# Kernel optimization log

Measured on AMD Instinct MI355X. Metric: run time of the kernel, lower is better.

## Reference

```python
import jax, jax.numpy as jnp
import numpy as np

B, TIN, NB, H, SOUT, R, G = 64, 49, 24, 384, 10, 2, 5  # batch, in_frames, bones, hidden, out_frames, rec_steps, gates(i,fs,ft,o,c)


def setup_inputs() -> dict:
    key = jax.random.key(0)
    ks = jax.random.split(key, 9)
    s = 1.0 / np.sqrt(H)  # scaled init so gates don't saturate (original uses randn)
    return {
        "hidden_states": jax.random.normal(ks[0], (B, TIN, NB, H), jnp.float32),
        "cell_states": jax.random.normal(ks[1], (B, TIN, NB, H), jnp.float32),
        "global_t_state": jax.random.normal(ks[2], (B, NB, H), jnp.float32),
        "global_s_state": jax.random.normal(ks[3], (B, TIN, H), jnp.float32),
        "p": jax.random.normal(ks[4], (B, SOUT, NB, H), jnp.float32),
        # per (rec_step, bone) cell weights: x / h_temporal / h_spatial projections for 5 gates
        "U": jax.random.normal(ks[5], (R, NB, G, H, H), jnp.float32) * s,
        "Wt": jax.random.normal(ks[6], (R, NB, G, H, H), jnp.float32) * s,
        "Ws": jax.random.normal(ks[7], (R, NB, G, H, H), jnp.float32) * s,
        "b": jax.random.normal(ks[8], (R, NB, G, H), jnp.float32) * s,
    }


def _cell(Ub, Wtb, Wsb, bb, x, ht, hs, ct, cs):
    # Ub/Wtb/Wsb: [G,H,H], bb: [G,H]; x/ht/hs/ct/cs: [B,H]
    g = (jnp.einsum('bh,ghk->bgk', x, Ub)
         + jnp.einsum('bh,ghk->bgk', ht, Wtb)
         + jnp.einsum('bh,ghk->bgk', hs, Wsb) + bb)
    i_n = jax.nn.sigmoid(g[:, 0])
    f_s = jax.nn.sigmoid(g[:, 1])
    f_t = jax.nn.sigmoid(g[:, 2])
    o_n = jax.nn.sigmoid(g[:, 3])
    c_n = jnp.tanh(g[:, 4])
    c_h = i_n * c_n + f_t * ct + f_s * cs
    return o_n * jnp.tanh(c_h), c_h


def reference(hidden_states, cell_states, global_t_state, global_s_state, p, U, Wt, Ws, b):
    # rec step 0: h_t = h_s = hidden_states; rec step 1: h_t = cat(global_t, hidden), h_s = hidden
    h_t1 = jnp.concatenate([global_t_state[:, None], hidden_states], axis=1)
    hm = hidden_states.mean(axis=(1, 2))                    # [B,H] spatial boundary (bone 0) for both steps
    cm = cell_states.mean(axis=(1, 2))
    bound_h = jnp.stack([hm, hm])                            # [R,B,H]
    bound_c = jnp.stack([cm, cm])
    h_prev = jnp.stack([hidden_states.mean(1), h_t1.mean(1)])  # [R,B,NB,H] frame-0 row (bones 1:)
    c_prev = jnp.stack([cell_states.mean(1)] * 2)

    Un, Wtn, Wsn, bn = (jnp.swapaxes(a, 0, 1) for a in (U, Wt, Ws, b))  # [NB,R,...]

    def frame_step(carry, p_f):  # p_f: [NB,B,H]
        h_prev, c_prev = carry                              # [R,B,NB,H]
        hp_n = jnp.moveaxis(h_prev, 2, 0)                   # [NB,R,B,H]
        cp_n = jnp.moveaxis(c_prev, 2, 0)

        def bone_step(bc, xs):
            hl, cl = bc                                     # [R,B,H] left-neighbor (spatial) state
            Ub, Wtb, Wsb, bb, x0, hp, cp = xs
            h0, c0 = _cell(Ub[0], Wtb[0], Wsb[0], bb[0], x0, hp[0], hl[0], cp[0], cl[0])
            h1, c1 = _cell(Ub[1], Wtb[1], Wsb[1], bb[1], h0, hp[1], hl[1], cp[1], cl[1])
            hn = jnp.stack([h0, h1])
            cn = jnp.stack([c0, c1])
            return (hn, cn), (hn, cn)

        _, (hs_all, cs_all) = jax.lax.scan(
            bone_step, (bound_h, bound_c), (Un, Wtn, Wsn, bn, p_f, hp_n, cp_n))
        h_new = jnp.moveaxis(hs_all, 0, 2)                  # [R,B,NB,H]
        c_new = jnp.moveaxis(cs_all, 0, 2)
        return (h_new, c_new), (h_new[-1], c_new[-1])

    p_frames = jnp.transpose(p, (1, 2, 0, 3))               # [SOUT,NB,B,H]
    _, (h_out, c_out) = jax.lax.scan(frame_step, (h_prev, c_prev), p_frames)
    return jnp.moveaxis(h_out, 0, 1), jnp.moveaxis(c_out, 0, 1)  # [B,SOUT,NB,H] each
```

## Files before the change

### kernel.cpp

```cpp
#include <hip/hip_runtime.h>

#define BATCH 64
#define TIN   49
#define NB    24
#define HID   384
#define SOUT  10
#define NGATE 5

typedef __attribute__((ext_vector_type(4))) float f32x4;
typedef __attribute__((ext_vector_type(8))) short short8v;

__device__ __forceinline__ unsigned short f2bf(float f) {
    union { float f; unsigned u; } v; v.f = f;
    unsigned r = v.u + 0x7fffu + ((v.u >> 16) & 1u);
    return (unsigned short)(r >> 16);
}
__device__ __forceinline__ float bf2f(unsigned short h) {
    union { unsigned u; float f; } v; v.u = ((unsigned)h) << 16; return v.f;
}

#define NW3_BLK 4320
#define NP_BLK  23040
#define NM_BLK  576

__global__ __launch_bounds__(256) void prologue_kernel(
    const float* __restrict__ U, const float* __restrict__ Wt,
    const float* __restrict__ Ws, const float* __restrict__ p,
    const float* __restrict__ hid, const float* __restrict__ cel,
    const float* __restrict__ gt,
    unsigned short* __restrict__ wpack, unsigned short* __restrict__ pb,
    unsigned short* __restrict__ hp_b, float* __restrict__ cp_f)
{
    __shared__ unsigned short tile[64][390];
    int bx = blockIdx.x;
    if (bx < NW3_BLK) {
        int q = bx;
        int kb = q % 6; q /= 6;
        int m  = q % 3; q /= 3;
        int g  = q % 5; q /= 5;
        int cell = q;
        const float* W = (m == 0) ? U : (m == 1) ? Wt : Ws;
        const float* src = W + ((size_t)(cell * NGATE + g) * HID + kb * 64) * HID;
        int tid = threadIdx.x;
#pragma unroll
        for (int i = 0; i < 24; ++i) {
            int c = tid + i * 256;
            int row = c / 96, c4 = (c % 96) * 4;
            float4 v = *(const float4*)(src + (size_t)row * HID + c4);
            tile[row][c4 + 0] = f2bf(v.x);
            tile[row][c4 + 1] = f2bf(v.y);
            tile[row][c4 + 2] = f2bf(v.z);
            tile[row][c4 + 3] = f2bf(v.w);
        }
        __syncthreads();
        int lane = tid & 63, grp = tid >> 6;
#pragma unroll
        for (int uu = 0; uu < 12; ++uu) {
            int unit = grp * 12 + uu;
            int pair = unit & 1, kc2 = (unit >> 1) & 1, t32 = unit >> 2;
            int kl = kc2 * 32 + (lane >> 4) * 8;
            int cl = t32 * 32 + pair * 16 + (lane & 15);
            unsigned short o[8];
#pragma unroll
            for (int jj = 0; jj < 8; ++jj) o[jj] = tile[kl + jj][cl];
            int kc = m * 12 + kb * 2 + kc2;
            size_t dst = ((size_t)((cell * 12 + t32) * NGATE + g) * 72
                          + kc * 2 + pair) * 64 + lane;
            *(short8v*)(wpack + dst * 8) = *(const short8v*)o;
        }
    } else if (bx < NW3_BLK + NP_BLK) {
        size_t idx = (size_t)(bx - NW3_BLK) * 256 + threadIdx.x;
        int h = (int)(idx % HID);
        size_t q = idx / HID;
        int b = (int)(q % BATCH); q /= BATCH;
        int n = (int)(q % NB); q /= NB;
        int f = (int)q;
        pb[idx] = f2bf(p[((size_t)(b * SOUT + f) * NB + n) * HID + h]);
    } else {
        int idx = (bx - NW3_BLK - NP_BLK) * 256 + threadIdx.x;
        const int total4 = NB * BATCH * HID / 4;
        if (idx >= total4) return;
        const int H4 = HID / 4;
        int h = (idx % H4) * 4;
        int b = (idx / H4) % BATCH;
        int n = idx / (H4 * BATCH);
        const int fs4 = NB * HID / 4;
        const float4* ph = (const float4*)(hid + ((size_t)b * TIN * NB + n) * HID + h);
        const float4* pc = (const float4*)(cel + ((size_t)b * TIN * NB + n) * HID + h);
        float sh[4] = {0,0,0,0}, sc[4] = {0,0,0,0};
        for (int t = 0; t < TIN; ++t) {
            float4 vh = ph[(size_t)t * fs4];
            float4 vc = pc[(size_t)t * fs4];
            sh[0] += vh.x; sh[1] += vh.y; sh[2] += vh.z; sh[3] += vh.w;
            sc[0] += vc.x; sc[1] += vc.y; sc[2] += vc.z; sc[3] += vc.w;
        }
        float4 g4 = *(const float4*)(gt + ((size_t)b * NB + n) * HID + h);
        const float* g_ = (const float*)&g4;
        unsigned short o0[4], o1[4];
        float c0[4];
#pragma unroll
        for (int j = 0; j < 4; ++j) {
            o0[j] = f2bf(sh[j] / TIN);
            o1[j] = f2bf((g_[j] + sh[j]) / (TIN + 1));
            c0[j] = sc[j] / TIN;
        }
        size_t base = (size_t)idx * 4;
        const size_t tot = (size_t)NB * BATCH * HID;
        *(uint2*)(hp_b + base)       = *(const uint2*)o0;
        *(uint2*)(hp_b + tot + base) = *(const uint2*)o1;
        *(float4*)(cp_f + base)       = make_float4(c0[0], c0[1], c0[2], c0[3]);
        *(float4*)(cp_f + tot + base) = make_float4(c0[0], c0[1], c0[2], c0[3]);
    }
}

__global__ void init_bounds_kernel(const unsigned short* __restrict__ hp_b,
                                   const float* __restrict__ cp_f,
                                   unsigned short* __restrict__ bh_b,
                                   float* __restrict__ bc_f) {
    int idx = blockIdx.x * blockDim.x + threadIdx.x;
    if (idx >= BATCH * HID) return;
    float sh = 0.f, sc = 0.f;
    for (int n = 0; n < NB; ++n) {
        sh += bf2f(hp_b[(size_t)n * BATCH * HID + idx]);
        sc += cp_f[(size_t)n * BATCH * HID + idx];
    }
    bh_b[idx] = f2bf(sh / NB);
    bc_f[idx] = sc / NB;
}

union SMem {
    unsigned short A[3][64][392];
    float gl[3][NGATE][64][35];
};

__global__ __launch_bounds__(960) void cell_fused_kernel(
    int d, int A0,
    const unsigned short* __restrict__ pb,
    const unsigned short* __restrict__ wpack,
    const float* __restrict__ bias,
    const unsigned short* __restrict__ hp_b,
    const float* __restrict__ cp_f,
    const unsigned short* __restrict__ bh_b,
    const float* __restrict__ bc_f,
    unsigned short* __restrict__ h_sl,
    float* __restrict__ c_sl,
    float* __restrict__ out)
{
    __shared__ SMem sm;

    int y = blockIdx.y;
    int rstep, dg;
    if (y < A0) { rstep = 0; dg = d; }
    else        { rstep = 1; dg = d - 1; y -= A0; }
    int lo = dg - (SOUT - 1); if (lo < 0) lo = 0;
    const int n = lo + y;
    const int f = dg - n;
    const int cur = dg & 1, prv = cur ^ 1;
    const int t = blockIdx.x;
    const int wv   = threadIdx.x >> 6;
    const int gate = wv % NGATE;
    const int m    = wv / NGATE;
    const int lane = threadIdx.x & 63;
    const int S = BATCH * HID;
    const int cell = rstep * NB + n;

    const unsigned short *xb, *htb, *hsb;
    const float *ctb, *csb;
    if (rstep == 0) {
        xb  = pb + (size_t)(f * NB + n) * S;
        htb = f ? h_sl + (size_t)((prv * 2 + 0) * NB + n) * S : hp_b + (size_t)n * S;
        hsb = n ? h_sl + (size_t)((prv * 2 + 0) * NB + n - 1) * S : bh_b;
        ctb = f ? c_sl + (size_t)((prv * 2 + 0) * NB + n) * S : cp_f + (size_t)n * S;
        csb = n ? c_sl + (size_t)((prv * 2 + 0) * NB + n - 1) * S : bc_f;
    } else {
        xb  = h_sl + (size_t)((cur * 2 + 0) * NB + n) * S;
        htb = f ? h_sl + (size_t)((prv * 2 + 1) * NB + n) * S
                : hp_b + (size_t)(NB + n) * S;
        hsb = n ? h_sl + (size_t)((prv * 2 + 1) * NB + n - 1) * S : bh_b;
        ctb = f ? c_sl + (size_t)((prv * 2 + 1) * NB + n) * S
                : cp_f + (size_t)(NB + n) * S;
        csb = n ? c_sl + (size_t)((prv * 2 + 1) * NB + n - 1) * S : bc_f;
    }

    const short8v* wp = (const short8v*)wpack
        + (size_t)((cell * 12 + t) * NGATE + gate) * (36 * 2 * 64);
    const short8v* wbm = wp + (size_t)(m * 24) * 64 + lane;

    const int eb = threadIdx.x & 63;
    const int ecq = (threadIdx.x >> 6) & 3;
    float4 cth[2], csh[2];
    if (threadIdx.x < 256) {
#pragma unroll
        for (int h = 0; h < 2; ++h) {
            int colg = t * 32 + h * 16 + ecq * 4;
            cth[h] = *(const float4*)(ctb + (size_t)eb * HID + colg);
            csh[h] = *(const float4*)(csb + (size_t)eb * HID + colg);
        }
    }

    const int tid = threadIdx.x;
    uint4 streg[12];
#pragma unroll
    for (int s = 0; s < 3; ++s) {
        const unsigned short* sp = (s == 0) ? xb : (s == 1) ? htb : hsb;
#pragma unroll
        for (int i = 0; i < 4; ++i) {
            int c = tid + i * 960;
            if (i < 3 || c < 3072) {
                int row = c / 48, cc = c - row * 48;
                streg[s * 4 + i] = *(const uint4*)(sp + (size_t)row * HID + cc * 8);
            }
        }
    }
#pragma unroll
    for (int s = 0; s < 3; ++s) {
#pragma unroll
        for (int i = 0; i < 4; ++i) {
            int c = tid + i * 960;
            if (i < 3 || c < 3072) {
                int row = c / 48, cc = c - row * 48;
                *(uint4*)&sm.A[s][row][cc * 8] = streg[s * 4 + i];
            }
        }
    }

    short8v bufB[3][2];
#pragma unroll
    for (int j = 0; j < 3; ++j) {
        bufB[j][0] = wbm[(size_t)j * 128];
        bufB[j][1] = wbm[(size_t)j * 128 + 64];
    }
    __syncthreads();

    f32x4 acc[2][4];
#pragma unroll
    for (int pr = 0; pr < 2; ++pr)
#pragma unroll
        for (int q = 0; q < 4; ++q) acc[pr][q] = (f32x4){0, 0, 0, 0};

    const int arow = lane & 15;
    const int akg  = (lane >> 4) * 8;

#pragma unroll
    for (int j = 0; j < 12; ++j) {
        const int koff = j * 32 + akg;
        short8v a[4];
#pragma unroll
        for (int q = 0; q < 4; ++q)
            a[q] = *(const short8v*)&sm.A[m][arow + q * 16][koff];
        const int sl = j % 3;
#pragma unroll
        for (int q = 0; q < 4; ++q) {
            acc[0][q] = __builtin_amdgcn_mfma_f32_16x16x32_bf16(a[q], bufB[sl][0], acc[0][q], 0, 0, 0);
            acc[1][q] = __builtin_amdgcn_mfma_f32_16x16x32_bf16(a[q], bufB[sl][1], acc[1][q], 0, 0, 0);
        }
        if (j < 9) {
            bufB[sl][0] = wbm[(size_t)(j + 3) * 128];
            bufB[sl][1] = wbm[(size_t)(j + 3) * 128 + 64];
        }
    }
    __syncthreads();

#pragma unroll
    for (int pr = 0; pr < 2; ++pr)
#pragma unroll
        for (int q = 0; q < 4; ++q)
#pragma unroll
            for (int i = 0; i < 4; ++i)
                sm.gl[m][gate][q * 16 + (lane >> 4) * 4 + i][pr * 16 + (lane & 15)]
                    = acc[pr][q][i];
    __syncthreads();

    if (threadIdx.x < 256) {
        size_t dbase = (size_t)((cur * 2 + rstep) * NB + n) * S + (size_t)eb * HID;
        const float* bbase = bias + (size_t)cell * NGATE * HID;
#pragma unroll
        for (int h = 0; h < 2; ++h) {
            int cloc = h * 16 + ecq * 4;
            int colg = t * 32 + cloc;
            const float* ct_ = (const float*)&cth[h];
            const float* cs_ = (const float*)&csh[h];
            float hv4[4], ch4[4];
            unsigned short hb4[4];
#pragma unroll
            for (int cc = 0; cc < 4; ++cc) {
                int c = cloc + cc;
                float gi  = sm.gl[0][0][eb][c] + sm.gl[1][0][eb][c] + sm.gl[2][0][eb][c] + bbase[0 * HID + colg + cc];
                float gfs = sm.gl[0][1][eb][c] + sm.gl[1][1][eb][c] + sm.gl[2][1][eb][c] + bbase[1 * HID + colg + cc];
                float gft = sm.gl[0][2][eb][c] + sm.gl[1][2][eb][c] + sm.gl[2][2][eb][c] + bbase[2 * HID + colg + cc];
                float go  = sm.gl[0][3][eb][c] + sm.gl[1][3][eb][c] + sm.gl[2][3][eb][c] + bbase[3 * HID + colg + cc];
                float gc  = sm.gl[0][4][eb][c] + sm.gl[1][4][eb][c] + sm.gl[2][4][eb][c] + bbase[4 * HID + colg + cc];
                float i_n = 1.f / (1.f + __expf(-gi));
                float f_s = 1.f / (1.f + __expf(-gfs));
                float f_t = 1.f / (1.f + __expf(-gft));
                float o_n = 1.f / (1.f + __expf(-go));
                float c_n = tanhf(gc);
                float ch  = i_n * c_n + f_t * ct_[cc] + f_s * cs_[cc];
                float hv  = o_n * tanhf(ch);
                hv4[cc] = hv; ch4[cc] = ch; hb4[cc] = f2bf(hv);
            }
            *(uint2*)(h_sl + dbase + colg) = *(const uint2*)hb4;
            *(float4*)(c_sl + dbase + colg) = make_float4(ch4[0], ch4[1], ch4[2], ch4[3]);
            if (rstep == 1) {
                size_t o = ((size_t)(eb * SOUT + f) * NB + n) * HID + colg;
                *(float4*)(out + o) = make_float4(hv4[0], hv4[1], hv4[2], hv4[3]);
                *(float4*)(out + (size_t)BATCH * SOUT * NB * HID + o)
                    = make_float4(ch4[0], ch4[1], ch4[2], ch4[3]);
            }
        }
    }
}

extern "C" void kernel_launch(void* const* d_in, const int* in_sizes, int n_in,
                              void* d_out, int out_size, void* d_ws, size_t ws_size,
                              hipStream_t stream) {
    const float* hid  = (const float*)d_in[0];
    const float* cel  = (const float*)d_in[1];
    const float* gt   = (const float*)d_in[2];
    const float* p    = (const float*)d_in[4];
    const float* U    = (const float*)d_in[5];
    const float* Wt   = (const float*)d_in[6];
    const float* Ws   = (const float*)d_in[7];
    const float* bias = (const float*)d_in[8];
    float* out = (float*)d_out;

    char* cur_ = (char*)d_ws;
    auto carve = [&](size_t bytes) -> void* {
        void* r = cur_; cur_ += (bytes + 255) & ~(size_t)255; return r;
    };
    const size_t NPBH = (size_t)NB * BATCH * HID;
    unsigned short* wpack = (unsigned short*)carve((size_t)13271040 * 16);
    unsigned short* pb    = (unsigned short*)carve((size_t)SOUT * NB * BATCH * HID * 2);
    unsigned short* hp_b  = (unsigned short*)carve(2 * NPBH * 2);
    float*          cp_f  = (float*)carve(2 * NPBH * 4);
    unsigned short* bh_b  = (unsigned short*)carve((size_t)BATCH * HID * 2);
    float*          bc_f  = (float*)carve((size_t)BATCH * HID * 4);
    unsigned short* h_sl  = (unsigned short*)carve(4 * NPBH * 2);
    float*          c_sl  = (float*)carve(4 * NPBH * 4);

    prologue_kernel<<<NW3_BLK + NP_BLK + NM_BLK, 256, 0, stream>>>(
        U, Wt, Ws, p, hid, cel, gt, wpack, pb, hp_b, cp_f);
    init_bounds_kernel<<<(BATCH * HID + 255) / 256, 256, 0, stream>>>(
        hp_b, cp_f, bh_b, bc_f);

    auto cnt = [](int dg) {
        int lo = dg - (SOUT - 1); if (lo < 0) lo = 0;
        int hi = (dg < NB - 1) ? dg : NB - 1;
        return hi - lo + 1;
    };
    for (int d = 0; d < SOUT + NB; ++d) {
        int A0 = (d <= SOUT + NB - 2) ? cnt(d) : 0;
        int A1 = (d >= 1) ? cnt(d - 1) : 0;
        dim3 grid(12, A0 + A1);
        cell_fused_kernel<<<grid, 960, 0, stream>>>(d, A0, pb, wpack, bias,
                                                    hp_b, cp_f, bh_b, bc_f,
                                                    h_sl, c_sl, out);
    }
}
```

Before: 1.249 ms.

## Process frame pairs per launch with intra-grid atomic barrier and narrower column tiles

Each block now handles two consecutive output frames of a cell, using a per-cell atomic counter spin-wait so all 24 column tiles finish frame f0 before any of them reads its h_t for frame f1. This roughly halves the number of wavefront kernel launches, from 34 to 29 here with pairs on a shorter diagonal. Tiles shrink to 16 columns so there are twice as many blocks per cell. State buffers become full per-frame storage instead of ping-pong slices. The spin-wait relies on all 24 blocks of a cell being co-resident, which risks deadlock. The narrower tiles halve MFMA work per A-tile load, so shared-memory staging costs more relative to compute.

```diff
diff --git a/kernel.cpp b/kernel.cpp
--- a/kernel.cpp
+++ b/kernel.cpp
@@ -6,6 +6,8 @@
 #define HID   384
 #define SOUT  10
 #define NGATE 5
+#define FPAIR 5
+#define TILE  24
 
 typedef __attribute__((ext_vector_type(4))) float f32x4;
 typedef __attribute__((ext_vector_type(8))) short short8v;
@@ -128,13 +130,18 @@
     bc_f[idx] = sc / NB;
 }
 
-union SMem {
+__global__ void reset_scnt(int* scnt) {
+    int i = blockIdx.x * 256 + threadIdx.x;
+    if (i < 2 * NB * FPAIR) scnt[i] = 0;
+}
+
+union SMemP {
     unsigned short A[3][64][392];
-    float gl[3][NGATE][64][35];
+    float gl[3][NGATE][64][17];
 };
 
-__global__ __launch_bounds__(960) void cell_fused_kernel(
-    int d, int A0,
+__global__ __launch_bounds__(960) void cell_pair_kernel(
+    int sd, int A0,
     const unsigned short* __restrict__ pb,
     const unsigned short* __restrict__ wpack,
     const float* __restrict__ bias,
@@ -142,154 +149,126 @@
     const float* __restrict__ cp_f,
     const unsigned short* __restrict__ bh_b,
     const float* __restrict__ bc_f,
-    unsigned short* __restrict__ h_sl,
-    float* __restrict__ c_sl,
-    float* __restrict__ out)
+    unsigned short* __restrict__ h_st,
+    float* __restrict__ c_st,
+    float* __restrict__ out,
+    int* __restrict__ scnt)
 {
-    __shared__ SMem sm;
-
-    int y = blockIdx.y;
-    int rstep, dg;
-    if (y < A0) { rstep = 0; dg = d; }
-    else        { rstep = 1; dg = d - 1; y -= A0; }
-    int lo = dg - (SOUT - 1); if (lo < 0) lo = 0;
-    const int n = lo + y;
-    const int f = dg - n;
-    const int cur = dg & 1, prv = cur ^ 1;
-    const int t = blockIdx.x;
-    const int wv   = threadIdx.x >> 6;
-    const int gate = wv % NGATE;
-    const int m    = wv / NGATE;
-    const int lane = threadIdx.x & 63;
+    __shared__ SMemP sm;
+
+    int y = (int)blockIdx.x / TILE;
+    const int t = (int)blockIdx.x % TILE;
+    int r, sdg;
+    if (y < A0) { r = 0; sdg = sd; }
+    else        { r = 1; sdg = sd - 1; y -= A0; }
+    int lo = sdg - (FPAIR - 1); if (lo < 0) lo = 0;
+    const int n  = lo + y;
+    const int fp = sdg - n;
+    const int f0 = fp * 2, f1 = f0 + 1;
+    const int cell = r * NB + n;
     const int S = BATCH * HID;
-    const int cell = rstep * NB + n;
-
-    const unsigned short *xb, *htb, *hsb;
-    const float *ctb, *csb;
-    if (rstep == 0) {
-        xb  = pb + (size_t)(f * NB + n) * S;
-        htb = f ? h_sl + (size_t)((prv * 2 + 0) * NB + n) * S : hp_b + (size_t)n * S;
-        hsb = n ? h_sl + (size_t)((prv * 2 + 0) * NB + n - 1) * S : bh_b;
-        ctb = f ? c_sl + (size_t)((prv * 2 + 0) * NB + n) * S : cp_f + (size_t)n * S;
-        csb = n ? c_sl + (size_t)((prv * 2 + 0) * NB + n - 1) * S : bc_f;
-    } else {
-        xb  = h_sl + (size_t)((cur * 2 + 0) * NB + n) * S;
-        htb = f ? h_sl + (size_t)((prv * 2 + 1) * NB + n) * S
-                : hp_b + (size_t)(NB + n) * S;
-        hsb = n ? h_sl + (size_t)((prv * 2 + 1) * NB + n - 1) * S : bh_b;
-        ctb = f ? c_sl + (size_t)((prv * 2 + 1) * NB + n) * S
-                : cp_f + (size_t)(NB + n) * S;
-        csb = n ? c_sl + (size_t)((prv * 2 + 1) * NB + n - 1) * S : bc_f;
-    }
-
-    const short8v* wp = (const short8v*)wpack
-        + (size_t)((cell * 12 + t) * NGATE + gate) * (36 * 2 * 64);
-    const short8v* wbm = wp + (size_t)(m * 24) * 64 + lane;
-
-    const int eb = threadIdx.x & 63;
-    const int ecq = (threadIdx.x >> 6) & 3;
-    float4 cth[2], csh[2];
-    if (threadIdx.x < 256) {
-#pragma unroll
-        for (int h = 0; h < 2; ++h) {
-            int colg = t * 32 + h * 16 + ecq * 4;
-            cth[h] = *(const float4*)(ctb + (size_t)eb * HID + colg);
-            csh[h] = *(const float4*)(csb + (size_t)eb * HID + colg);
-        }
-    }
-
     const int tid = threadIdx.x;
+    const int wv = tid >> 6, gate = wv % NGATE, m = wv / NGATE, lane = tid & 63;
+
+    auto hX = [&](int rr, int nn, int ff) -> size_t {
+        return (size_t)((rr * NB + nn) * SOUT + ff) * S;
+    };
+
+    const unsigned short *xbA, *htA, *hsA, *xbB, *htB, *hsB;
+    const float *ctA, *csA, *csB;
+    xbA = (r == 0) ? pb + (size_t)(f0 * NB + n) * S : h_st + hX(0, n, f0);
+    htA = f0 ? h_st + hX(r, n, f0 - 1) : hp_b + (size_t)cell * S;
+    hsA = n  ? h_st + hX(r, n - 1, f0) : bh_b;
+    ctA = f0 ? c_st + hX(r, n, f0 - 1) : cp_f + (size_t)cell * S;
+    csA = n  ? c_st + hX(r, n - 1, f0) : bc_f;
+    xbB = (r == 0) ? pb + (size_t)(f1 * NB + n) * S : h_st + hX(0, n, f1);
+    htB = h_st + hX(r, n, f0);
+    hsB = n  ? h_st + hX(r, n - 1, f1) : bh_b;
+    csB = n  ? c_st + hX(r, n - 1, f1) : bc_f;
+
+    const short8v* wbm = (const short8v*)wpack
+        + (size_t)((cell * 12 + (t >> 1)) * NGATE + gate) * (72 * 64)
+        + (size_t)((m * 12) * 2 + (t & 1)) * 64 + lane;
+
+    const int eb = tid & 63;
+    const int ecq = (tid >> 6) & 3;
+    const int colg = t * 16 + ecq * 4;
+
+    float4 ctA4, csA4;
+    if (tid < 256) {
+        ctA4 = *(const float4*)(ctA + (size_t)eb * HID + colg);
+        csA4 = *(const float4*)(csA + (size_t)eb * HID + colg);
+    }
+
     uint4 streg[12];
-#pragma unroll
-    for (int s = 0; s < 3; ++s) {
-        const unsigned short* sp = (s == 0) ? xb : (s == 1) ? htb : hsb;
+    auto LD1 = [&](const unsigned short* src, int slot) {
 #pragma unroll
         for (int i = 0; i < 4; ++i) {
             int c = tid + i * 960;
             if (i < 3 || c < 3072) {
                 int row = c / 48, cc = c - row * 48;
-                streg[s * 4 + i] = *(const uint4*)(sp + (size_t)row * HID + cc * 8);
-            }
-        }
-    }
-#pragma unroll
-    for (int s = 0; s < 3; ++s) {
+                streg[slot * 4 + i] = *(const uint4*)(src + (size_t)row * HID + cc * 8);
+            }
+        }
+    };
+    auto WR1 = [&](int s, int slot) {
 #pragma unroll
         for (int i = 0; i < 4; ++i) {
             int c = tid + i * 960;
             if (i < 3 || c < 3072) {
                 int row = c / 48, cc = c - row * 48;
-                *(uint4*)&sm.A[s][row][cc * 8] = streg[s * 4 + i];
-            }
-        }
-    }
-
-    short8v bufB[3][2];
-#pragma unroll
-    for (int j = 0; j < 3; ++j) {
-        bufB[j][0] = wbm[(size_t)j * 128];
-        bufB[j][1] = wbm[(size_t)j * 128 + 64];
-    }
-    __syncthreads();
-
-    f32x4 acc[2][4];
-#pragma unroll
-    for (int pr = 0; pr < 2; ++pr)
-#pragma unroll
-        for (int q = 0; q < 4; ++q) acc[pr][q] = (f32x4){0, 0, 0, 0};
-
-    const int arow = lane & 15;
-    const int akg  = (lane >> 4) * 8;
-
-#pragma unroll
-    for (int j = 0; j < 12; ++j) {
-        const int koff = j * 32 + akg;
-        short8v a[4];
+                *(uint4*)&sm.A[s][row][cc * 8] = streg[slot * 4 + i];
+            }
+        }
+    };
+
+    const int arow = lane & 15, akg = (lane >> 4) * 8;
+
+    auto COMPUTE_GL = [&]() {
+        short8v bw0 = wbm[0], bw1 = wbm[128], bw2 = wbm[256];
+        f32x4 acc[4];
+#pragma unroll
+        for (int q = 0; q < 4; ++q) acc[q] = (f32x4){0, 0, 0, 0};
+#pragma unroll
+        for (int j = 0; j < 12; ++j) {
+            const int koff = j * 32 + akg;
+            short8v a[4];
+#pragma unroll
+            for (int q = 0; q < 4; ++q)
+                a[q] = *(const short8v*)&sm.A[m][arow + q * 16][koff];
+            short8v bw = (j % 3 == 0) ? bw0 : (j % 3 == 1) ? bw1 : bw2;
+#pragma unroll
+            for (int q = 0; q < 4; ++q)
+                acc[q] = __builtin_amdgcn_mfma_f32_16x16x32_bf16(a[q], bw, acc[q], 0, 0, 0);
+            if (j < 9) {
+                if (j % 3 == 0)      bw0 = wbm[(size_t)(j + 3) * 128];
+                else if (j % 3 == 1) bw1 = wbm[(size_t)(j + 3) * 128];
+                else                 bw2 = wbm[(size_t)(j + 3) * 128];
+            }
+        }
+        __syncthreads();
 #pragma unroll
         for (int q = 0; q < 4; ++q)
-            a[q] = *(const short8v*)&sm.A[m][arow + q * 16][koff];
-        const int sl = j % 3;
-#pragma unroll
-        for (int q = 0; q < 4; ++q) {
-            acc[0][q] = __builtin_amdgcn_mfma_f32_16x16x32_bf16(a[q], bufB[sl][0], acc[0][q], 0, 0, 0);
-            acc[1][q] = __builtin_amdgcn_mfma_f32_16x16x32_bf16(a[q], bufB[sl][1], acc[1][q], 0, 0, 0);
-        }
-        if (j < 9) {
-            bufB[sl][0] = wbm[(size_t)(j + 3) * 128];
-            bufB[sl][1] = wbm[(size_t)(j + 3) * 128 + 64];
-        }
-    }
-    __syncthreads();
-
-#pragma unroll
-    for (int pr = 0; pr < 2; ++pr)
-#pragma unroll
-        for (int q = 0; q < 4; ++q)
 #pragma unroll
             for (int i = 0; i < 4; ++i)
-                sm.gl[m][gate][q * 16 + (lane >> 4) * 4 + i][pr * 16 + (lane & 15)]
-                    = acc[pr][q][i];
-    __syncthreads();
-
-    if (threadIdx.x < 256) {
-        size_t dbase = (size_t)((cur * 2 + rstep) * NB + n) * S + (size_t)eb * HID;
-        const float* bbase = bias + (size_t)cell * NGATE * HID;
-#pragma unroll
-        for (int h = 0; h < 2; ++h) {
-            int cloc = h * 16 + ecq * 4;
-            int colg = t * 32 + cloc;
-            const float* ct_ = (const float*)&cth[h];
-            const float* cs_ = (const float*)&csh[h];
-            float hv4[4], ch4[4];
-            unsigned short hb4[4];
+                sm.gl[m][gate][q * 16 + (lane >> 4) * 4 + i][lane & 15] = acc[q][i];
+        __syncthreads();
+    };
+
+    float chKeep[4];
+    auto EPI = [&](const float* ct_, const float* cs_, int f, bool saveCt) {
+        if (tid < 256) {
+            const float* bb = bias + (size_t)cell * NGATE * HID + colg;
+            size_t db = hX(r, n, f) + (size_t)eb * HID + colg;
+            unsigned short hb4[4]; float hv4[4], ch4[4];
 #pragma unroll
             for (int cc = 0; cc < 4; ++cc) {
-                int c = cloc + cc;
-                float gi  = sm.gl[0][0][eb][c] + sm.gl[1][0][eb][c] + sm.gl[2][0][eb][c] + bbase[0 * HID + colg + cc];
-                float gfs = sm.gl[0][1][eb][c] + sm.gl[1][1][eb][c] + sm.gl[2][1][eb][c] + bbase[1 * HID + colg + cc];
-                float gft = sm.gl[0][2][eb][c] + sm.gl[1][2][eb][c] + sm.gl[2][2][eb][c] + bbase[2 * HID + colg + cc];
-                float go  = sm.gl[0][3][eb][c] + sm.gl[1][3][eb][c] + sm.gl[2][3][eb][c] + bbase[3 * HID + colg + cc];
-                float gc  = sm.gl[0][4][eb][c] + sm.gl[1][4][eb][c] + sm.gl[2][4][eb][c] + bbase[4 * HID + colg + cc];
+                int c = ecq * 4 + cc;
+                float gi  = sm.gl[0][0][eb][c] + sm.gl[1][0][eb][c] + sm.gl[2][0][eb][c] + bb[0 * HID + cc];
+                float gfs = sm.gl[0][1][eb][c] + sm.gl[1][1][eb][c] + sm.gl[2][1][eb][c] + bb[1 * HID + cc];
+                float gft = sm.gl[0][2][eb][c] + sm.gl[1][2][eb][c] + sm.gl[2][2][eb][c] + bb[2 * HID + cc];
+                float go  = sm.gl[0][3][eb][c] + sm.gl[1][3][eb][c] + sm.gl[2][3][eb][c] + bb[3 * HID + cc];
+                float gc  = sm.gl[0][4][eb][c] + sm.gl[1][4][eb][c] + sm.gl[2][4][eb][c] + bb[4 * HID + cc];
                 float i_n = 1.f / (1.f + __expf(-gi));
                 float f_s = 1.f / (1.f + __expf(-gfs));
                 float f_t = 1.f / (1.f + __expf(-gft));
@@ -298,17 +277,48 @@
                 float ch  = i_n * c_n + f_t * ct_[cc] + f_s * cs_[cc];
                 float hv  = o_n * tanhf(ch);
                 hv4[cc] = hv; ch4[cc] = ch; hb4[cc] = f2bf(hv);
-            }
-            *(uint2*)(h_sl + dbase + colg) = *(const uint2*)hb4;
-            *(float4*)(c_sl + dbase + colg) = make_float4(ch4[0], ch4[1], ch4[2], ch4[3]);
-            if (rstep == 1) {
+                if (saveCt) chKeep[cc] = ch;
+            }
+            *(uint2*)(h_st + db) = *(const uint2*)hb4;
+            *(float4*)(c_st + db) = make_float4(ch4[0], ch4[1], ch4[2], ch4[3]);
+            if (r == 1) {
                 size_t o = ((size_t)(eb * SOUT + f) * NB + n) * HID + colg;
                 *(float4*)(out + o) = make_float4(hv4[0], hv4[1], hv4[2], hv4[3]);
                 *(float4*)(out + (size_t)BATCH * SOUT * NB * HID + o)
                     = make_float4(ch4[0], ch4[1], ch4[2], ch4[3]);
             }
         }
-    }
+    };
+
+    LD1(xbA, 0); LD1(htA, 1); LD1(hsA, 2);
+    WR1(0, 0);  WR1(1, 1);  WR1(2, 2);
+    __syncthreads();
+    COMPUTE_GL();
+    EPI((const float*)&ctA4, (const float*)&csA4, f0, true);
+    __syncthreads();
+
+    const int sci = (r * NB + n) * FPAIR + fp;
+    if (tid == 0)
+        __hip_atomic_fetch_add(scnt + sci, 1, __ATOMIC_RELEASE,
+                               __HIP_MEMORY_SCOPE_AGENT);
+    LD1(xbB, 0); LD1(hsB, 2);
+    WR1(0, 0);  WR1(2, 2);
+    float4 csB4;
+    if (tid < 256) csB4 = *(const float4*)(csB + (size_t)eb * HID + colg);
+    if (tid == 0) {
+        while (__hip_atomic_load(scnt + sci, __ATOMIC_RELAXED,
+                                 __HIP_MEMORY_SCOPE_AGENT) < TILE)
+            __builtin_amdgcn_s_sleep(4);
+        int z = __hip_atomic_load(scnt + sci, __ATOMIC_ACQUIRE,
+                                  __HIP_MEMORY_SCOPE_AGENT);
+        asm volatile("" :: "s"(z));
+    }
+    __syncthreads();
+
+    LD1(htB, 1); WR1(1, 1);
+    __syncthreads();
+    COMPUTE_GL();
+    EPI(chKeep, (const float*)&csB4, f1, false);
 }
 
 extern "C" void kernel_launch(void* const* d_in, const int* in_sizes, int n_in,
@@ -335,25 +345,28 @@
     float*          cp_f  = (float*)carve(2 * NPBH * 4);
     unsigned short* bh_b  = (unsigned short*)carve((size_t)BATCH * HID * 2);
     float*          bc_f  = (float*)carve((size_t)BATCH * HID * 4);
-    unsigned short* h_sl  = (unsigned short*)carve(4 * NPBH * 2);
-    float*          c_sl  = (float*)carve(4 * NPBH * 4);
-
+    unsigned short* h_st  = (unsigned short*)carve((size_t)2 * NB * SOUT * BATCH * HID * 2);
+    float*          c_st  = (float*)carve((size_t)2 * NB * SOUT * BATCH * HID * 4);
+    int*            scnt  = (int*)carve(2 * NB * FPAIR * sizeof(int));
+
+    reset_scnt<<<1, 256, 0, stream>>>(scnt);
     prologue_kernel<<<NW3_BLK + NP_BLK + NM_BLK, 256, 0, stream>>>(
         U, Wt, Ws, p, hid, cel, gt, wpack, pb, hp_b, cp_f);
     init_bounds_kernel<<<(BATCH * HID + 255) / 256, 256, 0, stream>>>(
         hp_b, cp_f, bh_b, bc_f);
 
-    auto cnt = [](int dg) {
-        int lo = dg - (SOUT - 1); if (lo < 0) lo = 0;
-        int hi = (dg < NB - 1) ? dg : NB - 1;
+    auto cnt = [](int sdg) {
+        if (sdg < 0 || sdg > NB - 1 + FPAIR - 1) return 0;
+        int lo = sdg - (FPAIR - 1); if (lo < 0) lo = 0;
+        int hi = (sdg < NB - 1) ? sdg : NB - 1;
         return hi - lo + 1;
     };
-    for (int d = 0; d < SOUT + NB; ++d) {
-        int A0 = (d <= SOUT + NB - 2) ? cnt(d) : 0;
-        int A1 = (d >= 1) ? cnt(d - 1) : 0;
-        dim3 grid(12, A0 + A1);
-        cell_fused_kernel<<<grid, 960, 0, stream>>>(d, A0, pb, wpack, bias,
-                                                    hp_b, cp_f, bh_b, bc_f,
-                                                    h_sl, c_sl, out);
-    }
-}
+    for (int sd = 0; sd <= NB + FPAIR - 1; ++sd) {
+        int A0 = cnt(sd);
+        int A1 = cnt(sd - 1);
+        if (A0 + A1 == 0) continue;
+        cell_pair_kernel<<<TILE * (A0 + A1), 960, 0, stream>>>(
+            sd, A0, pb, wpack, bias, hp_b, cp_f, bh_b, bc_f,
+            h_st, c_st, out, scnt);
+    }
+}
```

After: 1.976 ms. +58.2%, slower.

## Spread weight packing and p conversion across the early wavefront launches

Applied to the files above, without the earlier changes.

The prologue now packs bf16 weights only for bones 0–1 of both recurrence steps, and converts only the first two output frames of p. The remaining weight packing, three bones per launch, and p conversion, one frame per launch, are appended as extra blocks to the diagonal cell_fused_kernel launches. Each piece is scheduled two diagonals before it is first needed. The intent is to fill the idle CUs during the early, narrow diagonals and take the large packing pass off the critical path. In exchange, the cell kernel takes more arguments, uses a larger shared-memory union, and correctness now depends on the ordering between launches.

```diff
diff --git a/kernel.cpp b/kernel.cpp
--- a/kernel.cpp
+++ b/kernel.cpp
@@ -19,9 +19,11 @@
     union { unsigned u; float f; } v; v.u = ((unsigned)h) << 16; return v.f;
 }
 
-#define NW3_BLK 4320
-#define NP_BLK  23040
-#define NM_BLK  576
+#define NWU_BLK 360
+#define NPU_BLK 4608
+#define NMU_BLK 576
+#define PACK_TOT 3960
+#define PB_BLKS  16
 
 __global__ __launch_bounds__(256) void prologue_kernel(
     const float* __restrict__ U, const float* __restrict__ Wt,
@@ -33,12 +35,11 @@
 {
     __shared__ unsigned short tile[64][390];
     int bx = blockIdx.x;
-    if (bx < NW3_BLK) {
-        int q = bx;
-        int kb = q % 6; q /= 6;
-        int m  = q % 3; q /= 3;
-        int g  = q % 5; q /= 5;
-        int cell = q;
+    if (bx < NWU_BLK) {
+        int c4i = bx / 90;
+        int cell = (c4i < 2) ? c4i : 22 + c4i;
+        int sub = bx % 90;
+        int kb = sub % 6, m = (sub / 6) % 3, g = sub / 18;
         const float* W = (m == 0) ? U : (m == 1) ? Wt : Ws;
         const float* src = W + ((size_t)(cell * NGATE + g) * HID + kb * 64) * HID;
         int tid = threadIdx.x;
@@ -68,8 +69,8 @@
                           + kc * 2 + pair) * 64 + lane;
             *(short8v*)(wpack + dst * 8) = *(const short8v*)o;
         }
-    } else if (bx < NW3_BLK + NP_BLK) {
-        size_t idx = (size_t)(bx - NW3_BLK) * 256 + threadIdx.x;
+    } else if (bx < NWU_BLK + NPU_BLK) {
+        size_t idx = (size_t)(bx - NWU_BLK) * 256 + threadIdx.x;
         int h = (int)(idx % HID);
         size_t q = idx / HID;
         int b = (int)(q % BATCH); q /= BATCH;
@@ -77,7 +78,7 @@
         int f = (int)q;
         pb[idx] = f2bf(p[((size_t)(b * SOUT + f) * NB + n) * HID + h]);
     } else {
-        int idx = (bx - NW3_BLK - NP_BLK) * 256 + threadIdx.x;
+        int idx = (bx - NWU_BLK - NPU_BLK) * 256 + threadIdx.x;
         const int total4 = NB * BATCH * HID / 4;
         if (idx >= total4) return;
         const int H4 = HID / 4;
@@ -131,12 +132,15 @@
 union SMem {
     unsigned short A[3][64][392];
     float gl[3][NGATE][64][35];
+    unsigned short tile3[3][64][390];
 };
 
 __global__ __launch_bounds__(960) void cell_fused_kernel(
-    int d, int A0,
-    const unsigned short* __restrict__ pb,
-    const unsigned short* __restrict__ wpack,
+    int d, int A0, int cellBlocks, int packBase, int packBlocks, int pbF,
+    const float* __restrict__ U, const float* __restrict__ Wt,
+    const float* __restrict__ Ws, const float* __restrict__ p,
+    unsigned short* __restrict__ pb,
+    unsigned short* __restrict__ wpack,
     const float* __restrict__ bias,
     const unsigned short* __restrict__ hp_b,
     const float* __restrict__ cp_f,
@@ -147,8 +151,75 @@
     float* __restrict__ out)
 {
     __shared__ SMem sm;
-
-    int y = blockIdx.y;
+    const int bx = (int)blockIdx.x;
+    const int tid = threadIdx.x;
+
+    if (bx >= cellBlocks) {
+        if (bx < cellBlocks + packBlocks) {
+            const int sub3 = tid >> 8;
+            const int stid = tid & 255;
+            int pt = packBase + (bx - cellBlocks) * 3 + sub3;
+            bool act = (sub3 < 3) && (pt < PACK_TOT);
+            int cell = 0, g = 0, m = 0, kb = 0;
+            const float* src = U;
+            if (act) {
+                int bone = 2 + pt / 180;
+                int srem = pt % 180;
+                cell = (srem / 90) * NB + bone;
+                int sub = srem % 90;
+                kb = sub % 6; m = (sub / 6) % 3; g = sub / 18;
+                const float* W = (m == 0) ? U : (m == 1) ? Wt : Ws;
+                src = W + ((size_t)(cell * NGATE + g) * HID + kb * 64) * HID;
+            }
+            if (act) {
+#pragma unroll
+                for (int i = 0; i < 24; ++i) {
+                    int c = stid + i * 256;
+                    int row = c / 96, c4 = (c % 96) * 4;
+                    float4 v = *(const float4*)(src + (size_t)row * HID + c4);
+                    sm.tile3[sub3][row][c4 + 0] = f2bf(v.x);
+                    sm.tile3[sub3][row][c4 + 1] = f2bf(v.y);
+                    sm.tile3[sub3][row][c4 + 2] = f2bf(v.z);
+                    sm.tile3[sub3][row][c4 + 3] = f2bf(v.w);
+                }
+            }
+            __syncthreads();
+            if (act) {
+                int lane = stid & 63, grp = stid >> 6;
+#pragma unroll
+                for (int uu = 0; uu < 12; ++uu) {
+                    int unit = grp * 12 + uu;
+                    int pair = unit & 1, kc2 = (unit >> 1) & 1, t32 = unit >> 2;
+                    int kl = kc2 * 32 + (lane >> 4) * 8;
+                    int cl = t32 * 32 + pair * 16 + (lane & 15);
+                    unsigned short o[8];
+#pragma unroll
+                    for (int jj = 0; jj < 8; ++jj) o[jj] = sm.tile3[sub3][kl + jj][cl];
+                    int kc = m * 12 + kb * 2 + kc2;
+                    size_t dst = ((size_t)((cell * 12 + t32) * NGATE + g) * 72
+                                  + kc * 2 + pair) * 64 + lane;
+                    *(short8v*)(wpack + dst * 8) = *(const short8v*)o;
+                }
+            }
+        } else {
+            const int f = pbF;
+            int wbase = (bx - cellBlocks - packBlocks) * 960 + tid;
+            for (int w = wbase; w < NB * BATCH * HID / 4; w += PB_BLKS * 960) {
+                int l = w * 4;
+                int n = l / (BATCH * HID);
+                int rem = l - n * (BATCH * HID);
+                int b = rem / HID;
+                int h = rem - b * HID;
+                float4 v = *(const float4*)(p + ((size_t)(b * SOUT + f) * NB + n) * HID + h);
+                unsigned short o[4] = { f2bf(v.x), f2bf(v.y), f2bf(v.z), f2bf(v.w) };
+                *(uint2*)(pb + (size_t)f * NB * BATCH * HID + l) = *(const uint2*)o;
+            }
+        }
+        return;
+    }
+
+    const int t = bx % 12;
+    int y = bx / 12;
     int rstep, dg;
     if (y < A0) { rstep = 0; dg = d; }
     else        { rstep = 1; dg = d - 1; y -= A0; }
@@ -156,11 +227,10 @@
     const int n = lo + y;
     const int f = dg - n;
     const int cur = dg & 1, prv = cur ^ 1;
-    const int t = blockIdx.x;
-    const int wv   = threadIdx.x >> 6;
+    const int wv   = tid >> 6;
     const int gate = wv % NGATE;
     const int m    = wv / NGATE;
-    const int lane = threadIdx.x & 63;
+    const int lane = tid & 63;
     const int S = BATCH * HID;
     const int cell = rstep * NB + n;
 
@@ -186,10 +256,10 @@
         + (size_t)((cell * 12 + t) * NGATE + gate) * (36 * 2 * 64);
     const short8v* wbm = wp + (size_t)(m * 24) * 64 + lane;
 
-    const int eb = threadIdx.x & 63;
-    const int ecq = (threadIdx.x >> 6) & 3;
+    const int eb = tid & 63;
+    const int ecq = (tid >> 6) & 3;
     float4 cth[2], csh[2];
-    if (threadIdx.x < 256) {
+    if (tid < 256) {
 #pragma unroll
         for (int h = 0; h < 2; ++h) {
             int colg = t * 32 + h * 16 + ecq * 4;
@@ -198,7 +268,6 @@
         }
     }
 
-    const int tid = threadIdx.x;
     uint4 streg[12];
 #pragma unroll
     for (int s = 0; s < 3; ++s) {
@@ -236,7 +305,7 @@
 #pragma unroll
     for (int pr = 0; pr < 2; ++pr)
 #pragma unroll
-        for (int q = 0; q < 4; ++q) acc[pr][q] = (f32x4){0, 0, 0, 0};
+        for (int q2 = 0; q2 < 4; ++q2) acc[pr][q2] = (f32x4){0, 0, 0, 0};
 
     const int arow = lane & 15;
     const int akg  = (lane >> 4) * 8;
@@ -246,13 +315,13 @@
         const int koff = j * 32 + akg;
         short8v a[4];
 #pragma unroll
-        for (int q = 0; q < 4; ++q)
-            a[q] = *(const short8v*)&sm.A[m][arow + q * 16][koff];
+        for (int q2 = 0; q2 < 4; ++q2)
+            a[q2] = *(const short8v*)&sm.A[m][arow + q2 * 16][koff];
         const int sl = j % 3;
 #pragma unroll
-        for (int q = 0; q < 4; ++q) {
-            acc[0][q] = __builtin_amdgcn_mfma_f32_16x16x32_bf16(a[q], bufB[sl][0], acc[0][q], 0, 0, 0);
-            acc[1][q] = __builtin_amdgcn_mfma_f32_16x16x32_bf16(a[q], bufB[sl][1], acc[1][q], 0, 0, 0);
+        for (int q2 = 0; q2 < 4; ++q2) {
+            acc[0][q2] = __builtin_amdgcn_mfma_f32_16x16x32_bf16(a[q2], bufB[sl][0], acc[0][q2], 0, 0, 0);
+            acc[1][q2] = __builtin_amdgcn_mfma_f32_16x16x32_bf16(a[q2], bufB[sl][1], acc[1][q2], 0, 0, 0);
         }
         if (j < 9) {
             bufB[sl][0] = wbm[(size_t)(j + 3) * 128];
@@ -264,14 +333,14 @@
 #pragma unroll
     for (int pr = 0; pr < 2; ++pr)
 #pragma unroll
-        for (int q = 0; q < 4; ++q)
+        for (int q2 = 0; q2 < 4; ++q2)
 #pragma unroll
             for (int i = 0; i < 4; ++i)
-                sm.gl[m][gate][q * 16 + (lane >> 4) * 4 + i][pr * 16 + (lane & 15)]
-                    = acc[pr][q][i];
+                sm.gl[m][gate][q2 * 16 + (lane >> 4) * 4 + i][pr * 16 + (lane & 15)]
+                    = acc[pr][q2][i];
     __syncthreads();
 
-    if (threadIdx.x < 256) {
+    if (tid < 256) {
         size_t dbase = (size_t)((cur * 2 + rstep) * NB + n) * S + (size_t)eb * HID;
         const float* bbase = bias + (size_t)cell * NGATE * HID;
 #pragma unroll
@@ -338,7 +407,7 @@
     unsigned short* h_sl  = (unsigned short*)carve(4 * NPBH * 2);
     float*          c_sl  = (float*)carve(4 * NPBH * 4);
 
-    prologue_kernel<<<NW3_BLK + NP_BLK + NM_BLK, 256, 0, stream>>>(
+    prologue_kernel<<<NWU_BLK + NPU_BLK + NMU_BLK, 256, 0, stream>>>(
         U, Wt, Ws, p, hid, cel, gt, wpack, pb, hp_b, cp_f);
     init_bounds_kernel<<<(BATCH * HID + 255) / 256, 256, 0, stream>>>(
         hp_b, cp_f, bh_b, bc_f);
@@ -351,9 +420,18 @@
     for (int d = 0; d < SOUT + NB; ++d) {
         int A0 = (d <= SOUT + NB - 2) ? cnt(d) : 0;
         int A1 = (d >= 1) ? cnt(d - 1) : 0;
-        dim3 grid(12, A0 + A1);
-        cell_fused_kernel<<<grid, 960, 0, stream>>>(d, A0, pb, wpack, bias,
-                                                    hp_b, cp_f, bh_b, bc_f,
-                                                    h_sl, c_sl, out);
-    }
-}
+        int cellBlocks = 12 * (A0 + A1);
+        int packBase = 540 * d;
+        int packTiles = (packBase < PACK_TOT)
+                        ? ((PACK_TOT - packBase < 540) ? (PACK_TOT - packBase) : 540)
+                        : 0;
+        int packBlocks = (packTiles + 2) / 3;
+        int pbF = d + 2;
+        int pbBlocks = (pbF <= SOUT - 1) ? PB_BLKS : 0;
+        int grid = cellBlocks + packBlocks + pbBlocks;
+        cell_fused_kernel<<<grid, 960, 0, stream>>>(
+            d, A0, cellBlocks, packBase, packBlocks, pbF,
+            U, Wt, Ws, p, pb, wpack, bias, hp_b, cp_f, bh_b, bc_f,
+            h_sl, c_sl, out);
+    }
+}
```

Measured after the change: 1.199 ms. -3.9%, faster.
